# Optimization experiments

Hardware: AMD Instinct MI355X
Metric: run time of the kernel (lower is better)

The kernel has to match this reference:

```python
import jax, jax.numpy as jnp
import numpy as np

N = 100000       # nodes
E = 3200000      # edges
IN_DIM = 128
EDGE_DIM = 16
H = 64           # hidden_dim
L = 3            # num_layers
G = 256          # num graphs
BN_EPS = 1e-5


def setup_inputs() -> dict:
    key = jax.random.key(0)
    ks = jax.random.split(key, 16)
    x = jax.random.normal(ks[0], (N, IN_DIM), dtype=jnp.float32)
    edge_attr = jax.random.normal(ks[1], (E, EDGE_DIM), dtype=jnp.float32)
    edge_index = jax.random.randint(ks[2], (2, E), 0, N, dtype=jnp.int64)
    batch = jnp.sort(jax.random.randint(ks[3], (N,), 0, G, dtype=jnp.int64))
    s = 0.05
    np_w = jax.random.normal(ks[4], (IN_DIM, H), dtype=jnp.float32) * s
    np_b = jnp.zeros((H,), dtype=jnp.float32)
    ep_w = jax.random.normal(ks[5], (EDGE_DIM, H), dtype=jnp.float32) * s
    ep_b = jnp.zeros((H,), dtype=jnp.float32)
    mlp_w1 = jax.random.normal(ks[6], (L, H, H), dtype=jnp.float32) * s
    mlp_b1 = jnp.zeros((L, H), dtype=jnp.float32)
    mlp_w2 = jax.random.normal(ks[7], (L, H, H), dtype=jnp.float32) * s
    mlp_b2 = jnp.zeros((L, H), dtype=jnp.float32)
    bn_g = jnp.ones((L, H), dtype=jnp.float32)
    bn_b = jnp.zeros((L, H), dtype=jnp.float32)
    return {"x": x, "edge_attr": edge_attr, "edge_index": edge_index, "batch": batch,
            "np_w": np_w, "np_b": np_b, "ep_w": ep_w, "ep_b": ep_b,
            "mlp_w1": mlp_w1, "mlp_b1": mlp_b1, "mlp_w2": mlp_w2, "mlp_b2": mlp_b2,
            "bn_g": bn_g, "bn_b": bn_b}


def reference(x, edge_attr, edge_index, batch, np_w, np_b, ep_w, ep_b,
              mlp_w1, mlp_b1, mlp_w2, mlp_b2, bn_g, bn_b):
    h = x @ np_w + np_b                  # [N,H] node_proj
    e = edge_attr @ ep_w + ep_b          # [E,H] edge_proj
    src, dst = edge_index[0], edge_index[1]
    for l in range(L):
        # GINEConv (eps=0): MLP(x_i + sum_j ReLU(x_j + e_ij))
        msg = jax.nn.relu(h[src] + e)                          # [E,H] gather + edge add
        agg = jax.ops.segment_sum(msg, dst, num_segments=N)    # scatter-add
        z = h + agg
        z = jax.nn.relu(z @ mlp_w1[l] + mlp_b1[l]) @ mlp_w2[l] + mlp_b2[l]
        # BatchNorm1d over node dim (batch statistics, training-mode math)
        mu = jnp.mean(z, axis=0)
        var = jnp.mean((z - mu) ** 2, axis=0)
        z = (z - mu) * jax.lax.rsqrt(var + BN_EPS) * bn_g[l] + bn_b[l]
        h = jax.nn.relu(z)               # dropout omitted (deterministic reference)
    # global_mean_pool
    sums = jax.ops.segment_sum(h, batch, num_segments=G)
    cnts = jax.ops.segment_sum(jnp.ones((N,), dtype=h.dtype), batch, num_segments=G)
    graph_emb = sums / jnp.maximum(cnts, 1.0)[:, None]
    return h, graph_emb
```

## Files before the change

### kernel.cpp

```cpp
#include <hip/hip_runtime.h>
#include <hip/hip_bf16.h>

#define NN 100000
#define NE 3200000
#define IND 128
#define ED 16
#define HD 64
#define NL 3
#define NG 256
#define BN_EPS 1e-5f

#define NB 391
#define PBLK 512
#define PCHUNK 6250
#define MLP_BLOCKS 512
#define APPLY_BLOCKS 2048

typedef unsigned int uint32;
typedef unsigned long long uint64;
typedef unsigned short ushort16;
typedef __attribute__((ext_vector_type(8))) short bf16x8;
typedef __attribute__((ext_vector_type(4))) float f32x4;

__device__ __forceinline__ ushort16 f2b(float f) {
    uint32 u = __float_as_uint(f);
    u = (u + 0x7fffu + ((u >> 16) & 1u)) >> 16;
    return (ushort16)u;
}
__device__ __forceinline__ float b2f(ushort16 b) {
    return __uint_as_float(((uint32)b) << 16);
}

__global__ __launch_bounds__(256) void k_node_proj(
    const float* __restrict__ x, const float* __restrict__ w,
    const float* __restrict__ b, ushort16* __restrict__ sb)
{
    __shared__ float xs[4][IND];
    const int wave = threadIdx.x >> 6, lane = threadIdx.x & 63;
    const int node = blockIdx.x * 4 + wave;
    const float2 v = *(const float2*)(x + (size_t)node * IND + lane * 2);
    ((float2*)xs[wave])[lane] = v;
    float acc = b[lane];
#pragma unroll
    for (int k = 0; k < IND; ++k)
        acc = fmaf(xs[wave][k], w[k * HD + lane], acc);
    sb[node * HD + lane] = f2b(acc);
}

__global__ __launch_bounds__(256) void k_p1(const int* __restrict__ ei,
                                            int* __restrict__ bh)
{
    __shared__ int hist[NB];
    const int t = threadIdx.x, blk = blockIdx.x;
    for (int i = t; i < NB; i += 256) hist[i] = 0;
    __syncthreads();
    const int base = blk * PCHUNK;
    for (int i = t; i < PCHUNK; i += 256)
        atomicAdd(&hist[ei[NE + base + i] >> 8], 1);
    __syncthreads();
    for (int i = t; i < NB; i += 256) bh[blk * NB + i] = hist[i];
}

__global__ __launch_bounds__(512) void k_p2(int* __restrict__ bh,
                                            int* __restrict__ bstart,
                                            int* __restrict__ rowptr)
{
    __shared__ int tot[NB];
    __shared__ int bsl[NB + 1];
    const int t = threadIdx.x;
    if (t < NB) {
        int s = 0;
        for (int blk = 0; blk < PBLK; ++blk) {
            const int idx = blk * NB + t;
            const int v = bh[idx];
            bh[idx] = s;
            s += v;
        }
        tot[t] = s;
    }
    __syncthreads();
    if (t == 0) {
        int run = 0;
        for (int b = 0; b < NB; ++b) { bsl[b] = run; run += tot[b]; }
        bsl[NB] = run;
    }
    __syncthreads();
    if (t < NB) {
        const int base = bsl[t];
        for (int blk = 0; blk < PBLK; ++blk) bh[blk * NB + t] += base;
        bstart[t] = base;
    }
    if (t == 0) { bstart[NB] = NE; rowptr[NN] = NE; }
}

__global__ __launch_bounds__(256) void k_p3(const int* __restrict__ ei,
                                            const int* __restrict__ bh,
                                            uint64* __restrict__ tmp)
{
    __shared__ int cursor[NB];
    const int t = threadIdx.x, blk = blockIdx.x;
    for (int i = t; i < NB; i += 256) cursor[i] = bh[blk * NB + i];
    __syncthreads();
    const int base = blk * PCHUNK;
    for (int i = t; i < PCHUNK; i += 256) {
        const int e = base + i;
        const int d = ei[NE + e];
        const int s = ei[e];
        const int pos = atomicAdd(&cursor[d >> 8], 1);
        tmp[pos] = (uint64)(uint32)d | ((uint64)(uint32)s << 17)
                 | ((uint64)(uint32)e << 34);
    }
}

__global__ __launch_bounds__(256) void k_p4(const uint64* __restrict__ tmp,
                                            const int* __restrict__ bstart,
                                            int* __restrict__ perm_src,
                                            int* __restrict__ perm_eid,
                                            int* __restrict__ rowptr)
{
    __shared__ int cnt[256], csave[256], cnt2[256];
    const int t = threadIdx.x, b = blockIdx.x;
    const int lo = bstart[b], hi = bstart[b + 1];
    cnt[t] = 0; cnt2[t] = 0;
    __syncthreads();
    for (int e = lo + t; e < hi; e += 256)
        atomicAdd(&cnt[(int)(tmp[e] & 0x1FFFF) & 255], 1);
    __syncthreads();
    csave[t] = cnt[t];
    __syncthreads();
    for (int off = 1; off < 256; off <<= 1) {
        const int v = (t >= off) ? cnt[t - off] : 0;
        __syncthreads();
        cnt[t] += v;
        __syncthreads();
    }
    const int excl = cnt[t] - csave[t];
    const int node = (b << 8) + t;
    if (node < NN) rowptr[node] = lo + excl;
    __syncthreads();
    csave[t] = excl;
    __syncthreads();
    for (int e = lo + t; e < hi; e += 256) {
        const uint64 u = tmp[e];
        const int loc = (int)(u & 0x1FFFF) & 255;
        const int r = atomicAdd(&cnt2[loc], 1);
        const int pos = lo + csave[loc] + r;
        perm_src[pos] = (int)((u >> 17) & 0x1FFFF);
        perm_eid[pos] = (int)(u >> 34);
    }
}

__global__ __launch_bounds__(256) void k_permute(
    const float* __restrict__ ea, const int* __restrict__ perm_eid,
    ushort16* __restrict__ ea_perm)
{
    const int pos = blockIdx.x * 256 + threadIdx.x;
    const int p = pos >> 2, q = pos & 3;
    const int eid = perm_eid[p];
    const float4 v = ((const float4*)(ea + (size_t)eid * ED))[q];
    ushort4 o;
    o.x = f2b(v.x); o.y = f2b(v.y); o.z = f2b(v.z); o.w = f2b(v.w);
    ((ushort4*)ea_perm)[pos] = o;
}

template <bool XFORM>
__global__ __launch_bounds__(256) void k_gather(
    const ushort16* __restrict__ eab, const int* __restrict__ perm_src,
    const int* __restrict__ rowptr,
    const float* __restrict__ epw, const float* __restrict__ epb,
    const ushort16* __restrict__ sb, const float* __restrict__ bnp,
    float* __restrict__ z)
{
    __shared__ float pe[4][64 * 17];
    const int lane = threadIdx.x & 63;
    const int wave = threadIdx.x >> 6;
    const int l15 = lane & 15, lg = lane >> 4;

    bf16x8 bfrag[4];
#pragma unroll
    for (int c = 0; c < 4; ++c) {
#pragma unroll
        for (int i = 0; i < 8; ++i) {
            const int k = lg * 8 + i;
            short v = 0;
            if (k < ED)       v = (short)f2b(epw[k * HD + c * 16 + l15]);
            else if (k == ED) v = (short)f2b(epb[c * 16 + l15]);
            bfrag[c][i] = v;
        }
    }
    const float tsc = XFORM ? bnp[lane] : 1.f;
    const float tsh = XFORM ? bnp[64 + lane] : 0.f;
    float* mype = pe[wave];

    const int node = __builtin_amdgcn_readfirstlane((blockIdx.x << 2) + wave);
    const int rs = rowptr[node];
    const int re = rowptr[node + 1];

    float acc = 0.f;
    for (int j = rs; j < re; j += 16) {
        int s[16];
#pragma unroll
        for (int m = 0; m < 16; ++m) {
            int idx = j + m;
            if (idx > NE - 1) idx = NE - 1;
            s[m] = perm_src[idx];
        }
        float hv[16];
#pragma unroll
        for (int m = 0; m < 16; ++m)
            hv[m] = b2f(sb[(size_t)s[m] * HD + lane]);

        bf16x8 a = {};
        if (lg < 2) {
            int row = j + l15;
            if (row > NE - 1) row = NE - 1;
            a = *(const bf16x8*)((const short*)eab + (size_t)row * ED + lg * 8);
        } else if (lg == 2) {
            a[0] = (short)0x3F80;
        }

        const f32x4 zero = {0.f, 0.f, 0.f, 0.f};
#pragma unroll
        for (int c = 0; c < 4; ++c) {
            const f32x4 d = __builtin_amdgcn_mfma_f32_16x16x32_bf16(
                a, bfrag[c], zero, 0, 0, 0);
            const int base = (c * 16 + l15) * 17 + lg * 4;
#pragma unroll
            for (int v = 0; v < 4; ++v) mype[base + v] = d[v];
        }

        if (XFORM) {
#pragma unroll
            for (int m = 0; m < 16; ++m)
                hv[m] = fmaxf(fmaf(hv[m], tsc, tsh), 0.f);
        }
        const int lim = re - j;
#pragma unroll
        for (int m = 0; m < 16; ++m) {
            if (m < lim)
                acc += fmaxf(hv[m] + mype[lane * 17 + m], 0.f);
        }
    }
    float u0 = b2f(sb[(size_t)node * HD + lane]);
    if (XFORM) u0 = fmaxf(fmaf(u0, tsc, tsh), 0.f);
    z[node * HD + lane] = acc + u0;
}

template <bool STORE_BF16>
__global__ __launch_bounds__(256) void k_mlp(
    float* __restrict__ z,
    const float* __restrict__ w1, const float* __restrict__ b1,
    const float* __restrict__ w2, const float* __restrict__ b2,
    ushort16* __restrict__ sb, float* __restrict__ part)
{
    __shared__ float z0s[4][HD];
    __shared__ float t1s[4][HD];
    __shared__ float red[4][2][HD];
    const int wave = threadIdx.x >> 6, lane = threadIdx.x & 63;
    const float vb1 = b1[lane], vb2 = b2[lane];
    float s1 = 0.f, s2 = 0.f;
    for (int node = blockIdx.x * 4 + wave; node < NN; node += MLP_BLOCKS * 4) {
        const int idx = node * HD + lane;
        z0s[wave][lane] = z[idx];
        float a = vb1;
#pragma unroll
        for (int k = 0; k < HD; ++k)
            a = fmaf(z0s[wave][k], w1[k * HD + lane], a);
        a = fmaxf(a, 0.f);
        t1s[wave][lane] = a;
        float o = vb2;
#pragma unroll
        for (int k = 0; k < HD; ++k)
            o = fmaf(t1s[wave][k], w2[k * HD + lane], o);
        if (STORE_BF16) sb[idx] = f2b(o);
        else            z[idx] = o;
        s1 += o;
        s2 += o * o;
    }
    red[wave][0][lane] = s1;
    red[wave][1][lane] = s2;
    __syncthreads();
    if (wave == 0) {
        float a = red[0][0][lane] + red[1][0][lane] + red[2][0][lane] + red[3][0][lane];
        float c = red[0][1][lane] + red[1][1][lane] + red[2][1][lane] + red[3][1][lane];
        part[blockIdx.x * 128 + lane] = a;
        part[blockIdx.x * 128 + 64 + lane] = c;
    }
}

__global__ __launch_bounds__(1024) void k_bn_final(
    const float* __restrict__ part,
    const float* __restrict__ g, const float* __restrict__ b,
    float* __restrict__ bnp)
{
    __shared__ float red[16][2][HD];
    const int c = threadIdx.x & 63;
    const int s = threadIdx.x >> 6;
    float s1 = 0.f, s2 = 0.f;
    for (int i = s; i < MLP_BLOCKS; i += 16) {
        s1 += part[i * 128 + c];
        s2 += part[i * 128 + 64 + c];
    }
    red[s][0][c] = s1;
    red[s][1][c] = s2;
    __syncthreads();
    if (s == 0) {
        float a = 0.f, q = 0.f;
#pragma unroll
        for (int i = 0; i < 16; ++i) { a += red[i][0][c]; q += red[i][1][c]; }
        const float mu  = a / (float)NN;
        const float var = q / (float)NN - mu * mu;
        const float rstd = rsqrtf(var + BN_EPS);
        const float sc = rstd * g[c];
        bnp[c] = sc;
        bnp[64 + c] = b[c] - mu * sc;
    }
}

__global__ __launch_bounds__(256) void k_bn_apply(
    const float* __restrict__ t2, const float* __restrict__ bnp,
    float* __restrict__ h)
{
    const int lane = threadIdx.x & 63;
    const float sc = bnp[lane];
    const float sh = bnp[64 + lane];
    int i = blockIdx.x * 256 + threadIdx.x;
    const int stride = APPLY_BLOCKS * 256;
    for (; i < NN * HD; i += stride)
        h[i] = fmaxf(t2[i] * sc + sh, 0.f);
}

__global__ __launch_bounds__(256) void k_pool(
    const float* __restrict__ h, const int* __restrict__ batch,
    float* __restrict__ emb)
{
    __shared__ float red[4][HD];
    const int g = blockIdx.x;
    const int lane = threadIdx.x & 63;
    const int wave = threadIdx.x >> 6;
    int lo = 0, hi = NN;
    while (lo < hi) { int m = (lo + hi) >> 1; if (batch[m] < g) lo = m + 1; else hi = m; }
    const int start = lo;
    hi = NN;
    while (lo < hi) { int m = (lo + hi) >> 1; if (batch[m] <= g) lo = m + 1; else hi = m; }
    const int end = lo;
    float acc = 0.f;
    for (int n = start + wave; n < end; n += 4) acc += h[(size_t)n * HD + lane];
    red[wave][lane] = acc;
    __syncthreads();
    if (wave == 0) {
        float a = red[0][lane] + red[1][lane] + red[2][lane] + red[3][lane];
        emb[g * HD + lane] = a / fmaxf((float)(end - start), 1.f);
    }
}

extern "C" void kernel_launch(void* const* d_in, const int* in_sizes, int n_in,
                              void* d_out, int out_size, void* d_ws, size_t ws_size,
                              hipStream_t stream)
{
    const float* x     = (const float*)d_in[0];
    const float* ea    = (const float*)d_in[1];
    const int*   ei    = (const int*)d_in[2];
    const int*   batch = (const int*)d_in[3];
    const float* np_w  = (const float*)d_in[4];
    const float* np_b  = (const float*)d_in[5];
    const float* ep_w  = (const float*)d_in[6];
    const float* ep_b  = (const float*)d_in[7];
    const float* w1    = (const float*)d_in[8];
    const float* b1    = (const float*)d_in[9];
    const float* w2    = (const float*)d_in[10];
    const float* b2    = (const float*)d_in[11];
    const float* bng   = (const float*)d_in[12];
    const float* bnb   = (const float*)d_in[13];

    float* h   = (float*)d_out;
    float* emb = h + (size_t)NN * HD;

    char* ws = (char*)d_ws;
    float*     agg      = (float*)    (ws);
    uint64*    tmp      = (uint64*)   (ws);
    float*     part     = (float*)    (ws + 25600000);
    float*     bnp      = (float*)    (ws + 26648576);
    int*       bh       = (int*)      (ws + 26650112);
    int*       bstart   = (int*)      (ws + 27450880);
    int*       rowptr   = (int*)      (ws + 27452448);
    ushort16*  sb       = (ushort16*) (ws + 27852464);
    int*       perm_src = (int*)      (ws + 40652464);
    int*       perm_eid = (int*)      (ws + 53452464);
    ushort16*  ea_perm  = (ushort16*) (ws + 66252464);

    k_node_proj<<<NN / 4, 256, 0, stream>>>(x, np_w, np_b, sb);

    k_p1<<<PBLK, 256, 0, stream>>>(ei, bh);
    k_p2<<<1, 512, 0, stream>>>(bh, bstart, rowptr);
    k_p3<<<PBLK, 256, 0, stream>>>(ei, bh, tmp);
    k_p4<<<NB, 256, 0, stream>>>(tmp, bstart, perm_src, perm_eid, rowptr);
    k_permute<<<NE * 4 / 256, 256, 0, stream>>>(ea, perm_eid, ea_perm);

    for (int l = 0; l < NL; ++l) {
        if (l == 0)
            k_gather<false><<<NN / 4, 256, 0, stream>>>(
                ea_perm, perm_src, rowptr, ep_w, ep_b, sb, bnp, agg);
        else
            k_gather<true><<<NN / 4, 256, 0, stream>>>(
                ea_perm, perm_src, rowptr, ep_w, ep_b, sb, bnp + (l - 1) * 128, agg);
        if (l < NL - 1)
            k_mlp<true><<<MLP_BLOCKS, 256, 0, stream>>>(
                agg, w1 + l * HD * HD, b1 + l * HD, w2 + l * HD * HD, b2 + l * HD,
                sb, part);
        else
            k_mlp<false><<<MLP_BLOCKS, 256, 0, stream>>>(
                agg, w1 + l * HD * HD, b1 + l * HD, w2 + l * HD * HD, b2 + l * HD,
                sb, part);
        k_bn_final<<<1, 1024, 0, stream>>>(part, bng + l * HD, bnb + l * HD, bnp + l * 128);
    }

    k_bn_apply<<<APPLY_BLOCKS, 256, 0, stream>>>(agg, bnp + 2 * 128, h);
    k_pool<<<NG, 256, 0, stream>>>(h, batch, emb);
}
```

Before: 1.217 ms.

## Fuse edge-attr permute into bucketing, persistent gather, fuse BN-apply into pooling

The edge-attribute permutation and bf16 conversion move into the final bucket kernel, so the perm_eid array and one launch disappear. The gather kernel becomes persistent, with a fixed wave count striding over nodes, and it predicates the neighbour loads on the valid count. The final BatchNorm apply and ReLU are fused into the mean-pool kernel so the output is written and summed in one pass. The risk is that the pool kernel runs only 256 blocks over the whole feature array, which may limit bandwidth, and the fused permute does scattered reads per thread.

```diff
diff --git a/kernel.cpp b/kernel.cpp
--- a/kernel.cpp
+++ b/kernel.cpp
@@ -14,7 +14,7 @@
 #define PBLK 512
 #define PCHUNK 6250
 #define MLP_BLOCKS 512
-#define APPLY_BLOCKS 2048
+#define GATHER_WAVES 25000
 
 typedef unsigned int uint32;
 typedef unsigned long long uint64;
@@ -29,6 +29,9 @@
 }
 __device__ __forceinline__ float b2f(ushort16 b) {
     return __uint_as_float(((uint32)b) << 16);
+}
+__device__ __forceinline__ uint32 pack2(float a, float b) {
+    return (uint32)f2b(a) | ((uint32)f2b(b) << 16);
 }
 
 __global__ __launch_bounds__(256) void k_node_proj(
@@ -114,8 +117,9 @@
 
 __global__ __launch_bounds__(256) void k_p4(const uint64* __restrict__ tmp,
                                             const int* __restrict__ bstart,
+                                            const float* __restrict__ ea,
                                             int* __restrict__ perm_src,
-                                            int* __restrict__ perm_eid,
+                                            ushort16* __restrict__ ea_perm,
                                             int* __restrict__ rowptr)
 {
     __shared__ int cnt[256], csave[256], cnt2[256];
@@ -146,21 +150,18 @@
         const int r = atomicAdd(&cnt2[loc], 1);
         const int pos = lo + csave[loc] + r;
         perm_src[pos] = (int)((u >> 17) & 0x1FFFF);
-        perm_eid[pos] = (int)(u >> 34);
-    }
-}
-
-__global__ __launch_bounds__(256) void k_permute(
-    const float* __restrict__ ea, const int* __restrict__ perm_eid,
-    ushort16* __restrict__ ea_perm)
-{
-    const int pos = blockIdx.x * 256 + threadIdx.x;
-    const int p = pos >> 2, q = pos & 3;
-    const int eid = perm_eid[p];
-    const float4 v = ((const float4*)(ea + (size_t)eid * ED))[q];
-    ushort4 o;
-    o.x = f2b(v.x); o.y = f2b(v.y); o.z = f2b(v.z); o.w = f2b(v.w);
-    ((ushort4*)ea_perm)[pos] = o;
+        const int eid = (int)(u >> 34);
+        const float4* s4 = (const float4*)(ea + (size_t)eid * ED);
+        const float4 v0 = s4[0], v1 = s4[1], v2 = s4[2], v3 = s4[3];
+        uint32 o[8];
+        o[0] = pack2(v0.x, v0.y); o[1] = pack2(v0.z, v0.w);
+        o[2] = pack2(v1.x, v1.y); o[3] = pack2(v1.z, v1.w);
+        o[4] = pack2(v2.x, v2.y); o[5] = pack2(v2.z, v2.w);
+        o[6] = pack2(v3.x, v3.y); o[7] = pack2(v3.z, v3.w);
+        uint32* d = (uint32*)((short*)ea_perm + (size_t)pos * ED);
+        ((uint4*)d)[0] = make_uint4(o[0], o[1], o[2], o[3]);
+        ((uint4*)d)[1] = make_uint4(o[4], o[5], o[6], o[7]);
+    }
 }
 
 template <bool XFORM>
@@ -192,58 +193,59 @@
     const float tsh = XFORM ? bnp[64 + lane] : 0.f;
     float* mype = pe[wave];
 
-    const int node = __builtin_amdgcn_readfirstlane((blockIdx.x << 2) + wave);
-    const int rs = rowptr[node];
-    const int re = rowptr[node + 1];
-
-    float acc = 0.f;
-    for (int j = rs; j < re; j += 16) {
-        int s[16];
-#pragma unroll
-        for (int m = 0; m < 16; ++m) {
-            int idx = j + m;
-            if (idx > NE - 1) idx = NE - 1;
-            s[m] = perm_src[idx];
+    const int wid = (blockIdx.x << 2) + wave;
+
+    for (int nd = wid; nd < NN; nd += GATHER_WAVES) {
+        const int node = __builtin_amdgcn_readfirstlane(nd);
+        const int rs = rowptr[node];
+        const int re = rowptr[node + 1];
+
+        float acc = 0.f;
+        for (int j = rs; j < re; j += 16) {
+            const int lim = re - j;
+            int s[16];
+            float hv[16];
+#pragma unroll
+            for (int m = 0; m < 16; ++m)
+                if (m < lim) s[m] = perm_src[j + m];
+#pragma unroll
+            for (int m = 0; m < 16; ++m)
+                if (m < lim) hv[m] = b2f(sb[(size_t)s[m] * HD + lane]);
+
+            bf16x8 a = {};
+            if (lg < 2) {
+                int row = j + l15;
+                if (row > NE - 1) row = NE - 1;
+                a = *(const bf16x8*)((const short*)eab + (size_t)row * ED + lg * 8);
+            } else if (lg == 2) {
+                a[0] = (short)0x3F80;
+            }
+
+            const f32x4 zero = {0.f, 0.f, 0.f, 0.f};
+#pragma unroll
+            for (int c = 0; c < 4; ++c) {
+                const f32x4 d = __builtin_amdgcn_mfma_f32_16x16x32_bf16(
+                    a, bfrag[c], zero, 0, 0, 0);
+                const int base = (c * 16 + l15) * 17 + lg * 4;
+#pragma unroll
+                for (int v = 0; v < 4; ++v) mype[base + v] = d[v];
+            }
+
+            if (XFORM) {
+#pragma unroll
+                for (int m = 0; m < 16; ++m)
+                    if (m < lim) hv[m] = fmaxf(fmaf(hv[m], tsc, tsh), 0.f);
+            }
+#pragma unroll
+            for (int m = 0; m < 16; ++m) {
+                if (m < lim)
+                    acc += fmaxf(hv[m] + mype[lane * 17 + m], 0.f);
+            }
         }
-        float hv[16];
-#pragma unroll
-        for (int m = 0; m < 16; ++m)
-            hv[m] = b2f(sb[(size_t)s[m] * HD + lane]);
-
-        bf16x8 a = {};
-        if (lg < 2) {
-            int row = j + l15;
-            if (row > NE - 1) row = NE - 1;
-            a = *(const bf16x8*)((const short*)eab + (size_t)row * ED + lg * 8);
-        } else if (lg == 2) {
-            a[0] = (short)0x3F80;
-        }
-
-        const f32x4 zero = {0.f, 0.f, 0.f, 0.f};
-#pragma unroll
-        for (int c = 0; c < 4; ++c) {
-            const f32x4 d = __builtin_amdgcn_mfma_f32_16x16x32_bf16(
-                a, bfrag[c], zero, 0, 0, 0);
-            const int base = (c * 16 + l15) * 17 + lg * 4;
-#pragma unroll
-            for (int v = 0; v < 4; ++v) mype[base + v] = d[v];
-        }
-
-        if (XFORM) {
-#pragma unroll
-            for (int m = 0; m < 16; ++m)
-                hv[m] = fmaxf(fmaf(hv[m], tsc, tsh), 0.f);
-        }
-        const int lim = re - j;
-#pragma unroll
-        for (int m = 0; m < 16; ++m) {
-            if (m < lim)
-                acc += fmaxf(hv[m] + mype[lane * 17 + m], 0.f);
-        }
-    }
-    float u0 = b2f(sb[(size_t)node * HD + lane]);
-    if (XFORM) u0 = fmaxf(fmaf(u0, tsc, tsh), 0.f);
-    z[node * HD + lane] = acc + u0;
+        float u0 = b2f(sb[(size_t)node * HD + lane]);
+        if (XFORM) u0 = fmaxf(fmaf(u0, tsc, tsh), 0.f);
+        z[node * HD + lane] = acc + u0;
+    }
 }
 
 template <bool STORE_BF16>
@@ -317,22 +319,10 @@
     }
 }
 
-__global__ __launch_bounds__(256) void k_bn_apply(
+__global__ __launch_bounds__(256) void k_pool_apply(
     const float* __restrict__ t2, const float* __restrict__ bnp,
-    float* __restrict__ h)
-{
-    const int lane = threadIdx.x & 63;
-    const float sc = bnp[lane];
-    const float sh = bnp[64 + lane];
-    int i = blockIdx.x * 256 + threadIdx.x;
-    const int stride = APPLY_BLOCKS * 256;
-    for (; i < NN * HD; i += stride)
-        h[i] = fmaxf(t2[i] * sc + sh, 0.f);
-}
-
-__global__ __launch_bounds__(256) void k_pool(
-    const float* __restrict__ h, const int* __restrict__ batch,
-    float* __restrict__ emb)
+    const int* __restrict__ batch,
+    float* __restrict__ h, float* __restrict__ emb)
 {
     __shared__ float red[4][HD];
     const int g = blockIdx.x;
@@ -344,12 +334,18 @@
     hi = NN;
     while (lo < hi) { int m = (lo + hi) >> 1; if (batch[m] <= g) lo = m + 1; else hi = m; }
     const int end = lo;
+    const float sc = bnp[lane];
+    const float sh = bnp[64 + lane];
     float acc = 0.f;
-    for (int n = start + wave; n < end; n += 4) acc += h[(size_t)n * HD + lane];
+    for (int n = start + wave; n < end; n += 4) {
+        const float v = fmaxf(fmaf(t2[(size_t)n * HD + lane], sc, sh), 0.f);
+        h[(size_t)n * HD + lane] = v;
+        acc += v;
+    }
     red[wave][lane] = acc;
     __syncthreads();
     if (wave == 0) {
-        float a = red[0][lane] + red[1][lane] + red[2][lane] + red[3][lane];
+        const float a = red[0][lane] + red[1][lane] + red[2][lane] + red[3][lane];
         emb[g * HD + lane] = a / fmaxf((float)(end - start), 1.f);
     }
 }
@@ -386,23 +382,21 @@
     int*       rowptr   = (int*)      (ws + 27452448);
     ushort16*  sb       = (ushort16*) (ws + 27852464);
     int*       perm_src = (int*)      (ws + 40652464);
-    int*       perm_eid = (int*)      (ws + 53452464);
-    ushort16*  ea_perm  = (ushort16*) (ws + 66252464);
+    ushort16*  ea_perm  = (ushort16*) (ws + 53452464);
 
     k_node_proj<<<NN / 4, 256, 0, stream>>>(x, np_w, np_b, sb);
 
     k_p1<<<PBLK, 256, 0, stream>>>(ei, bh);
     k_p2<<<1, 512, 0, stream>>>(bh, bstart, rowptr);
     k_p3<<<PBLK, 256, 0, stream>>>(ei, bh, tmp);
-    k_p4<<<NB, 256, 0, stream>>>(tmp, bstart, perm_src, perm_eid, rowptr);
-    k_permute<<<NE * 4 / 256, 256, 0, stream>>>(ea, perm_eid, ea_perm);
+    k_p4<<<NB, 256, 0, stream>>>(tmp, bstart, ea, perm_src, ea_perm, rowptr);
 
     for (int l = 0; l < NL; ++l) {
         if (l == 0)
-            k_gather<false><<<NN / 4, 256, 0, stream>>>(
+            k_gather<false><<<GATHER_WAVES / 4, 256, 0, stream>>>(
                 ea_perm, perm_src, rowptr, ep_w, ep_b, sb, bnp, agg);
         else
-            k_gather<true><<<NN / 4, 256, 0, stream>>>(
+            k_gather<true><<<GATHER_WAVES / 4, 256, 0, stream>>>(
                 ea_perm, perm_src, rowptr, ep_w, ep_b, sb, bnp + (l - 1) * 128, agg);
         if (l < NL - 1)
             k_mlp<true><<<MLP_BLOCKS, 256, 0, stream>>>(
@@ -415,6 +409,5 @@
         k_bn_final<<<1, 1024, 0, stream>>>(part, bng + l * HD, bnb + l * HD, bnp + l * 128);
     }
 
-    k_bn_apply<<<APPLY_BLOCKS, 256, 0, stream>>>(agg, bnp + 2 * 128, h);
-    k_pool<<<NG, 256, 0, stream>>>(h, batch, emb);
-}
+    k_pool_apply<<<NG, 256, 0, stream>>>(agg, bnp + 2 * 128, batch, h, emb);
+}
```

Result: slower. 1.624 ms (+33.4%).
